# Optimization experiments

Hardware: AMD Instinct MI355X
Metric: run time of the kernel (lower is better)

The kernel has to match this reference:

```python
import jax, jax.numpy as jnp
import numpy as np

B, S, H = 4, 2048, 2048

def setup_inputs() -> dict:
    key = jax.random.key(0)
    k1, k2, k3 = jax.random.split(key, 3)
    xav_qkv = float(np.sqrt(6.0 / (H + 3 * H)))
    xav_out = float(np.sqrt(6.0 / (H + H)))
    return {
        "hidden_states": jax.random.normal(k1, (B, S, H), dtype=jnp.float32),
        "w_qkv": jax.random.uniform(k2, (3 * H, H), minval=-xav_qkv, maxval=xav_qkv, dtype=jnp.float32),
        "b_qkv": jnp.zeros((3 * H,), dtype=jnp.float32),
        "w_out": jax.random.uniform(k3, (H, H), minval=-xav_out, maxval=xav_out, dtype=jnp.float32),
        "b_out": jnp.zeros((H,), dtype=jnp.float32),
    }

def reference(hidden_states, w_qkv, b_qkv, w_out, b_out):
    Bc, Sc, Hc = hidden_states.shape
    scaling = jnp.sqrt(jnp.asarray(Hc, hidden_states.dtype))
    # qkv projection: torch Linear is x @ W^T + b
    qkv = jnp.einsum('bsh,oh->bso', hidden_states, w_qkv) + b_qkv  # [B,S,3H]
    q, k, v = jnp.split(qkv, 3, axis=-1)  # each [B,S,H]
    scores = jnp.einsum('bqh,bkh->bqk', q, k) / scaling  # [B,S,S]
    probs = jax.nn.softmax(scores, axis=-1)
    context = jnp.einsum('bqk,bkh->bqh', probs, v)  # [B,S,H]
    out = jnp.einsum('bsh,oh->bso', context, w_out) + b_out
    return out
```

## Files before the change

### kernel.cpp

```cpp
#include <hip/hip_runtime.h>
#include <cstdint>

typedef _Float16 f16;
typedef __attribute__((ext_vector_type(8))) _Float16 f16x8;
typedef __attribute__((ext_vector_type(4))) _Float16 f16x4;
typedef __attribute__((ext_vector_type(4))) float f32x4;

typedef __attribute__((address_space(1))) void gvoid_t;
typedef __attribute__((address_space(3))) void lvoid_t;

__device__ __forceinline__ void async_copy16(void* lds, const void* g) {
  __builtin_amdgcn_global_load_lds((gvoid_t*)(uintptr_t)g, (lvoid_t*)lds, 16, 0, 0);
}

#define BARRIER()   __builtin_amdgcn_s_barrier()
#define SCHEDBAR()  __builtin_amdgcn_sched_barrier(0)
#define VMCNT(n)    do { SCHEDBAR(); asm volatile("s_waitcnt vmcnt(" #n ")"); SCHEDBAR(); } while (0)

#define MFMA16(a, b, c) __builtin_amdgcn_mfma_f32_16x16x32_f16((a), (b), (c), 0, 0, 0)

template<int OUT_F16>
__device__ __forceinline__ void gemm_body(const f16* __restrict__ Ab, int lda,
                                          const f16* __restrict__ Bb, int ldb,
                                          void* __restrict__ Cz, int ldc,
                                          const float* __restrict__ bias,
                                          float scale, int K)
{
  __shared__ f16 AH0a[8192]; __shared__ f16 AH0b[8192];
  __shared__ f16 AH1a[8192]; __shared__ f16 AH1b[8192];
  __shared__ f16 BH0a[8192]; __shared__ f16 BH0b[8192];
  __shared__ f16 BH1a[8192]; __shared__ f16 BH1b[8192];

  const int tid = threadIdx.x, lane = tid & 63, wave = tid >> 6;
  const int wr = wave >> 2, wc = wave & 3;
  const int l15 = lane & 15, lk = lane >> 4;

  int lin = blockIdx.y * gridDim.x + blockIdx.x;
  const int nxy = gridDim.x * gridDim.y;
  if ((nxy & 7) == 0) lin = (lin & 7) * (nxy >> 3) + (lin >> 3);
  const int bx = lin % gridDim.x, by = lin / gridDim.x;

  const long brow = (long)by * 256, bcol = (long)bx * 256;

  const int r0  = tid >> 3;
  const int gc8 = (tid & 7) ^ (r0 & 7);
  const int sdst = wave * 512;

  const f16* gAa = Ab + (brow + r0) * (long)lda + gc8 * 8;
  const f16* gAb = gAa + 128L * lda;
  const f16* gBa = Bb + (bcol + r0) * (long)ldb + gc8 * 8;
  const f16* gBb = gBa + 128L * ldb;

#define STG(BUF, G, LD, KOFF) { \
    async_copy16(BUF + sdst,        (G) + (KOFF)); \
    async_copy16(BUF + 4096 + sdst, (G) + 64L * (LD) + (KOFF)); }

  const f16* myA0 = wr ? AH0b : AH0a;
  const f16* myA1 = wr ? AH1b : AH1a;
  const f16* myB0 = (wc & 2) ? BH0b : BH0a;
  const f16* myB1 = (wc & 2) ? BH1b : BH1a;

  const int x8   = l15 & 7;
  const int cb0  = (lk ^ x8) * 8;
  const int cb1  = ((4 | lk) ^ x8) * 8;
  const int lbA  = l15 * 64;
  const int lbB  = ((wc & 1) * 64 + l15) * 64;

#define RDA4(SRC, MP) { \
    af[0] = *(const f16x8*)&(SRC)[lbA + (2*(MP))   * 1024 + cb0]; \
    af[1] = *(const f16x8*)&(SRC)[lbA + (2*(MP))   * 1024 + cb1]; \
    af[2] = *(const f16x8*)&(SRC)[lbA + (2*(MP)+1) * 1024 + cb0]; \
    af[3] = *(const f16x8*)&(SRC)[lbA + (2*(MP)+1) * 1024 + cb1]; }

#define RDB8(SRC) { \
    bf[0][0] = *(const f16x8*)&(SRC)[lbB + 0 * 1024 + cb0]; \
    bf[1][0] = *(const f16x8*)&(SRC)[lbB + 0 * 1024 + cb1]; \
    bf[0][1] = *(const f16x8*)&(SRC)[lbB + 1 * 1024 + cb0]; \
    bf[1][1] = *(const f16x8*)&(SRC)[lbB + 1 * 1024 + cb1]; \
    bf[0][2] = *(const f16x8*)&(SRC)[lbB + 2 * 1024 + cb0]; \
    bf[1][2] = *(const f16x8*)&(SRC)[lbB + 2 * 1024 + cb1]; \
    bf[0][3] = *(const f16x8*)&(SRC)[lbB + 3 * 1024 + cb0]; \
    bf[1][3] = *(const f16x8*)&(SRC)[lbB + 3 * 1024 + cb1]; }

#define CLUSTER(MP) { \
    __builtin_amdgcn_s_setprio(1); \
    _Pragma("unroll") \
    for (int n = 0; n < 4; ++n) { \
      f32x4 t = MFMA16(af[0], bf[0][n], acc[2*(MP)][n]); \
      acc[2*(MP)][n] = MFMA16(af[1], bf[1][n], t); \
    } \
    _Pragma("unroll") \
    for (int n = 0; n < 4; ++n) { \
      f32x4 t = MFMA16(af[2], bf[0][n], acc[2*(MP)+1][n]); \
      acc[2*(MP)+1][n] = MFMA16(af[3], bf[1][n], t); \
    } \
    __builtin_amdgcn_s_setprio(0); }

  f32x4 acc[8][4] = {};
  f16x8 af[4], bf[2][4];
  const int NIT = K >> 7;

  STG(BH0a, gBa, ldb, 0);  STG(BH0b, gBb, ldb, 0);
  STG(AH0a, gAa, lda, 0);  STG(AH0b, gAb, lda, 0);
  STG(BH1a, gBa, ldb, 64);
  VMCNT(2);
  BARRIER();

  for (int J = 0; J < NIT; ++J) {
    const long k1 = 128L * J + 64;
    const long k2 = 128L * J + 128;
    const long k3 = 128L * J + 192;
    const bool st = (J + 1 < NIT);

    RDB8(myB0); RDA4(myA0, 0);
    STG(BH1b, gBb, ldb, k1);
    CLUSTER(0);
    RDA4(myA0, 1);
    STG(AH1a, gAa, lda, k1);
    CLUSTER(1);
    BARRIER();

    RDA4(myA0, 2);
    STG(AH1b, gAb, lda, k1);
    CLUSTER(2);
    RDA4(myA0, 3);
    if (st) STG(BH0a, gBa, ldb, k2);
    CLUSTER(3);
    if (st) { VMCNT(2); } else { VMCNT(0); }
    BARRIER();

    RDB8(myB1); RDA4(myA1, 0);
    if (st) STG(BH0b, gBb, ldb, k2);
    CLUSTER(0);
    RDA4(myA1, 1);
    if (st) STG(AH0a, gAa, lda, k2);
    CLUSTER(1);
    BARRIER();

    RDA4(myA1, 2);
    if (st) STG(AH0b, gAb, lda, k2);
    CLUSTER(2);
    RDA4(myA1, 3);
    if (st) STG(BH1a, gBa, ldb, k3);
    CLUSTER(3);
    if (st) VMCNT(2);
    BARRIER();
  }

#pragma unroll
  for (int m = 0; m < 8; ++m) {
#pragma unroll
    for (int n = 0; n < 4; ++n) {
      const long col = bcol + wc * 64 + n * 16 + l15;
      const float bv = bias ? bias[col] : 0.0f;
#pragma unroll
      for (int j = 0; j < 4; ++j) {
        const long row = brow + wr * 128 + m * 16 + lk * 4 + j;
        const float v = acc[m][n][j] * scale + bv;
        if (OUT_F16)
          ((f16*)Cz)[row * (long)ldc + col] = (f16)v;
        else
          ((float*)Cz)[row * (long)ldc + col] = v;
      }
    }
  }
#undef STG
#undef RDA4
#undef RDB8
#undef CLUSTER
}

template<int OUT_F16>
__global__ __launch_bounds__(512, 2)
void gemm256(const f16* __restrict__ A, int lda, long sA,
             const f16* __restrict__ B, int ldb, long sB,
             void* __restrict__ Cv, int ldc, long sC,
             const float* __restrict__ bias, float scale, int K)
{
  const int z = blockIdx.z;
  void* Cz = OUT_F16 ? (void*)((f16*)Cv + (long)z * sC)
                     : (void*)((float*)Cv + (long)z * sC);
  gemm_body<OUT_F16>(A + (long)z * sA, lda, B + (long)z * sB, ldb,
                     Cz, ldc, bias, scale, K);
}

__global__ __launch_bounds__(512, 2)
void gemm_sv(const f16* __restrict__ QKV, const f16* __restrict__ Wouth,
             f16* __restrict__ SCH, f16* __restrict__ VWT, float inv_sqrt_h)
{
  const int z = blockIdx.z;
  const long sQ = 2048L * 6144, sS = 2048L * 2048;
  if (z < 4) {
    gemm_body<1>(QKV + z * sQ, 6144, QKV + 2048 + z * sQ, 6144,
                 SCH + z * sS, 2048, nullptr, inv_sqrt_h, 2048);
  } else {
    const int zz = z - 4;
    gemm_body<1>(Wouth, 2048, QKV + 4096 + zz * sQ, 6144,
                 VWT + zz * sS, 2048, nullptr, 1.0f, 2048);
  }
}

__global__ void cast_all(const float* __restrict__ x,     f16* __restrict__ xh,
                         const float* __restrict__ wq,    f16* __restrict__ wqh,
                         const float* __restrict__ wo,    f16* __restrict__ woh)
{
  const int b = blockIdx.x;
  const float* in; f16* out; long n; int b0, nb;
  if (b < 2048)      { in = x;  out = xh;  n = 16777216L; b0 = 0;    nb = 2048; }
  else if (b < 3584) { in = wq; out = wqh; n = 12582912L; b0 = 2048; nb = 1536; }
  else               { in = wo; out = woh; n = 4194304L;  b0 = 3584; nb = 512;  }
  long i = ((long)(b - b0) * 256 + threadIdx.x) * 4;
  const long stride = (long)nb * 256 * 4;
  for (; i < n; i += stride) {
    const float4 v = *reinterpret_cast<const float4*>(in + i);
    f16x4 h;
    h.x = (f16)v.x; h.y = (f16)v.y; h.z = (f16)v.z; h.w = (f16)v.w;
    *reinterpret_cast<f16x4*>(out + i) = h;
  }
}

__global__ __launch_bounds__(256)
void softmax_rows(f16* __restrict__ scores) {
  const long row = blockIdx.x;
  f16* s = scores + row * 2048;
  const int tid = threadIdx.x;
  const int lane = tid & 63;
  const int wave = tid >> 6;

  const f16x8 hv = *reinterpret_cast<const f16x8*>(s + tid * 8);
  float v[8];
  float sum = 0.f;
#pragma unroll
  for (int j = 0; j < 8; ++j) { v[j] = __expf((float)hv[j]); sum += v[j]; }
#pragma unroll
  for (int off = 32; off >= 1; off >>= 1) sum += __shfl_xor(sum, off);
  __shared__ float red[4];
  if (lane == 0) red[wave] = sum;
  __syncthreads();
  const float inv = 1.0f / (red[0] + red[1] + red[2] + red[3]);

  f16x8 h;
#pragma unroll
  for (int j = 0; j < 8; ++j) h[j] = (f16)(v[j] * inv);
  *reinterpret_cast<f16x8*>(s + tid * 8) = h;
}

extern "C" void kernel_launch(void* const* d_in, const int* in_sizes, int n_in,
                              void* d_out, int out_size, void* d_ws, size_t ws_size,
                              hipStream_t stream) {
  const float* x     = (const float*)d_in[0];
  const float* w_qkv = (const float*)d_in[1];
  const float* b_qkv = (const float*)d_in[2];
  const float* w_out = (const float*)d_in[3];
  const float* b_out = (const float*)d_in[4];
  float* out = (float*)d_out;

  char* ws = (char*)d_ws;
  f16*   Xh    = (f16*)(ws + 0);
  f16*   Wqkvh = (f16*)(ws + 33554432L);
  f16*   Wouth = (f16*)(ws + 58720256L);
  f16*   QKV   = (f16*)(ws + 67108864L);
  f16*   SCH   = (f16*)(ws + 167772160L);
  f16*   VWT   = (f16*)(ws + 234881024L);

  const float inv_sqrt_h = 0.022097086912079608f;

  cast_all<<<4096, 256, 0, stream>>>(x, Xh, w_qkv, Wqkvh, w_out, Wouth);

  gemm256<1><<<dim3(24, 32, 1), 512, 0, stream>>>(
      Xh, 2048, 0, Wqkvh, 2048, 0, QKV, 6144, 0, b_qkv, 1.0f, 2048);

  gemm_sv<<<dim3(8, 8, 8), 512, 0, stream>>>(QKV, Wouth, SCH, VWT, inv_sqrt_h);

  softmax_rows<<<8192, 256, 0, stream>>>(SCH);

  gemm256<0><<<dim3(8, 8, 4), 512, 0, stream>>>(
      SCH, 2048, 2048L * 2048, VWT, 2048, 2048L * 2048,
      out, 2048, 2048L * 2048, b_out, 1.0f, 2048);
}
```

Baseline: 433.8 us.

## Fuse softmax into score GEMM epilogue with atomic row sums and deferred normalization

```diff
diff --git a/kernel.cpp b/kernel.cpp
--- a/kernel.cpp
+++ b/kernel.cpp
@@ -19,18 +19,22 @@
 
 #define MFMA16(a, b, c) __builtin_amdgcn_mfma_f32_16x16x32_f16((a), (b), (c), 0, 0, 0)
 
-template<int OUT_F16>
-__device__ __forceinline__ void gemm_body(const f16* __restrict__ Ab, int lda,
+struct Smem {
+  f16 AH0a[8192]; f16 AH0b[8192];
+  f16 AH1a[8192]; f16 AH1b[8192];
+  f16 BH0a[8192]; f16 BH0b[8192];
+  f16 BH1a[8192]; f16 BH1b[8192];
+};
+
+template<int EPI>
+__device__ __forceinline__ void gemm_body(Smem& sm,
+                                          const f16* __restrict__ Ab, int lda,
                                           const f16* __restrict__ Bb, int ldb,
                                           void* __restrict__ Cz, int ldc,
                                           const float* __restrict__ bias,
+                                          float* __restrict__ rs,
                                           float scale, int K)
 {
-  __shared__ f16 AH0a[8192]; __shared__ f16 AH0b[8192];
-  __shared__ f16 AH1a[8192]; __shared__ f16 AH1b[8192];
-  __shared__ f16 BH0a[8192]; __shared__ f16 BH0b[8192];
-  __shared__ f16 BH1a[8192]; __shared__ f16 BH1b[8192];
-
   const int tid = threadIdx.x, lane = tid & 63, wave = tid >> 6;
   const int wr = wave >> 2, wc = wave & 3;
   const int l15 = lane & 15, lk = lane >> 4;
@@ -55,10 +59,10 @@
     async_copy16(BUF + sdst,        (G) + (KOFF)); \
     async_copy16(BUF + 4096 + sdst, (G) + 64L * (LD) + (KOFF)); }
 
-  const f16* myA0 = wr ? AH0b : AH0a;
-  const f16* myA1 = wr ? AH1b : AH1a;
-  const f16* myB0 = (wc & 2) ? BH0b : BH0a;
-  const f16* myB1 = (wc & 2) ? BH1b : BH1a;
+  const f16* myA0 = wr ? sm.AH0b : sm.AH0a;
+  const f16* myA1 = wr ? sm.AH1b : sm.AH1a;
+  const f16* myB0 = (wc & 2) ? sm.BH0b : sm.BH0a;
+  const f16* myB1 = (wc & 2) ? sm.BH1b : sm.BH1a;
 
   const int x8   = l15 & 7;
   const int cb0  = (lk ^ x8) * 8;
@@ -100,9 +104,9 @@
   f16x8 af[4], bf[2][4];
   const int NIT = K >> 7;
 
-  STG(BH0a, gBa, ldb, 0);  STG(BH0b, gBb, ldb, 0);
-  STG(AH0a, gAa, lda, 0);  STG(AH0b, gAb, lda, 0);
-  STG(BH1a, gBa, ldb, 64);
+  STG(sm.BH0a, gBa, ldb, 0);  STG(sm.BH0b, gBb, ldb, 0);
+  STG(sm.AH0a, gAa, lda, 0);  STG(sm.AH0b, gAb, lda, 0);
+  STG(sm.BH1a, gBa, ldb, 64);
   VMCNT(2);
   BARRIER();
 
@@ -113,35 +117,35 @@
     const bool st = (J + 1 < NIT);
 
     RDB8(myB0); RDA4(myA0, 0);
-    STG(BH1b, gBb, ldb, k1);
+    STG(sm.BH1b, gBb, ldb, k1);
     CLUSTER(0);
     RDA4(myA0, 1);
-    STG(AH1a, gAa, lda, k1);
+    STG(sm.AH1a, gAa, lda, k1);
     CLUSTER(1);
     BARRIER();
 
     RDA4(myA0, 2);
-    STG(AH1b, gAb, lda, k1);
+    STG(sm.AH1b, gAb, lda, k1);
     CLUSTER(2);
     RDA4(myA0, 3);
-    if (st) STG(BH0a, gBa, ldb, k2);
+    if (st) STG(sm.BH0a, gBa, ldb, k2);
     CLUSTER(3);
     if (st) { VMCNT(2); } else { VMCNT(0); }
     BARRIER();
 
     RDB8(myB1); RDA4(myA1, 0);
-    if (st) STG(BH0b, gBb, ldb, k2);
+    if (st) STG(sm.BH0b, gBb, ldb, k2);
     CLUSTER(0);
     RDA4(myA1, 1);
-    if (st) STG(AH0a, gAa, lda, k2);
+    if (st) STG(sm.AH0a, gAa, lda, k2);
     CLUSTER(1);
     BARRIER();
 
     RDA4(myA1, 2);
-    if (st) STG(AH0b, gAb, lda, k2);
+    if (st) STG(sm.AH0b, gAb, lda, k2);
     CLUSTER(2);
     RDA4(myA1, 3);
-    if (st) STG(BH1a, gBa, ldb, k3);
+    if (st) STG(sm.BH1a, gBa, ldb, k3);
     CLUSTER(3);
     if (st) VMCNT(2);
     BARRIER();
@@ -150,17 +154,30 @@
 #pragma unroll
   for (int m = 0; m < 8; ++m) {
 #pragma unroll
-    for (int n = 0; n < 4; ++n) {
-      const long col = bcol + wc * 64 + n * 16 + l15;
-      const float bv = bias ? bias[col] : 0.0f;
+    for (int j = 0; j < 4; ++j) {
+      const long row = brow + wr * 128 + m * 16 + lk * 4 + j;
+      float inv = 0.f, part = 0.f;
+      if (EPI == 3) inv = 1.0f / rs[row];
 #pragma unroll
-      for (int j = 0; j < 4; ++j) {
-        const long row = brow + wr * 128 + m * 16 + lk * 4 + j;
-        const float v = acc[m][n][j] * scale + bv;
-        if (OUT_F16)
-          ((f16*)Cz)[row * (long)ldc + col] = (f16)v;
-        else
-          ((float*)Cz)[row * (long)ldc + col] = v;
+      for (int n = 0; n < 4; ++n) {
+        const long col = bcol + wc * 64 + n * 16 + l15;
+        const float a = acc[m][n][j];
+        if (EPI == 1) {
+          ((f16*)Cz)[row * (long)ldc + col] = (f16)(a * scale + (bias ? bias[col] : 0.f));
+        } else if (EPI == 2) {
+          const float e = __expf(a * scale);
+          part += e;
+          ((f16*)Cz)[row * (long)ldc + col] = (f16)e;
+        } else {
+          ((float*)Cz)[row * (long)ldc + col] = a * inv + bias[col];
+        }
+      }
+      if (EPI == 2) {
+        part += __shfl_xor(part, 1, 16);
+        part += __shfl_xor(part, 2, 16);
+        part += __shfl_xor(part, 4, 16);
+        part += __shfl_xor(part, 8, 16);
+        if (l15 == 0) atomicAdd(&rs[row], part);
       }
     }
   }
@@ -170,41 +187,57 @@
 #undef CLUSTER
 }
 
-template<int OUT_F16>
 __global__ __launch_bounds__(512, 2)
-void gemm256(const f16* __restrict__ A, int lda, long sA,
-             const f16* __restrict__ B, int ldb, long sB,
-             void* __restrict__ Cv, int ldc, long sC,
-             const float* __restrict__ bias, float scale, int K)
-{
-  const int z = blockIdx.z;
-  void* Cz = OUT_F16 ? (void*)((f16*)Cv + (long)z * sC)
-                     : (void*)((float*)Cv + (long)z * sC);
-  gemm_body<OUT_F16>(A + (long)z * sA, lda, B + (long)z * sB, ldb,
-                     Cz, ldc, bias, scale, K);
+void gemm_qkv(const f16* __restrict__ Xh, const f16* __restrict__ Wqkvh,
+              f16* __restrict__ QKV, const float* __restrict__ b_qkv)
+{
+  __shared__ Smem sm;
+  gemm_body<1>(sm, Xh, 2048, Wqkvh, 2048, QKV, 6144, b_qkv, nullptr, 1.0f, 2048);
 }
 
 __global__ __launch_bounds__(512, 2)
 void gemm_sv(const f16* __restrict__ QKV, const f16* __restrict__ Wouth,
-             f16* __restrict__ SCH, f16* __restrict__ VWT, float inv_sqrt_h)
-{
+             f16* __restrict__ SCH, f16* __restrict__ VWT,
+             float* __restrict__ RS, float inv_sqrt_h)
+{
+  __shared__ Smem sm;
   const int z = blockIdx.z;
   const long sQ = 2048L * 6144, sS = 2048L * 2048;
   if (z < 4) {
-    gemm_body<1>(QKV + z * sQ, 6144, QKV + 2048 + z * sQ, 6144,
-                 SCH + z * sS, 2048, nullptr, inv_sqrt_h, 2048);
+    gemm_body<2>(sm, QKV + z * sQ, 6144, QKV + 2048 + z * sQ, 6144,
+                 SCH + z * sS, 2048, nullptr, RS + z * 2048, inv_sqrt_h, 2048);
   } else {
     const int zz = z - 4;
-    gemm_body<1>(Wouth, 2048, QKV + 4096 + zz * sQ, 6144,
-                 VWT + zz * sS, 2048, nullptr, 1.0f, 2048);
-  }
+    gemm_body<1>(sm, Wouth, 2048, QKV + 4096 + zz * sQ, 6144,
+                 VWT + zz * sS, 2048, nullptr, nullptr, 1.0f, 2048);
+  }
+}
+
+__global__ __launch_bounds__(512, 2)
+void gemm_out(const f16* __restrict__ SCH, const f16* __restrict__ VWT,
+              float* __restrict__ out, float* __restrict__ RS,
+              const float* __restrict__ b_out)
+{
+  __shared__ Smem sm;
+  const int z = blockIdx.z;
+  const long sS = 2048L * 2048;
+  gemm_body<3>(sm, SCH + z * sS, 2048, VWT + z * sS, 2048,
+               out + z * sS, 2048, b_out, RS + z * 2048, 1.0f, 2048);
 }
 
 __global__ void cast_all(const float* __restrict__ x,     f16* __restrict__ xh,
                          const float* __restrict__ wq,    f16* __restrict__ wqh,
-                         const float* __restrict__ wo,    f16* __restrict__ woh)
+                         const float* __restrict__ wo,    f16* __restrict__ woh,
+                         float* __restrict__ rs)
 {
   const int b = blockIdx.x;
+  if (b >= 4096) {
+    float4 z4 = {0.f, 0.f, 0.f, 0.f};
+    float* p = rs + (long)(b - 4096) * 2048 + threadIdx.x * 8;
+    *reinterpret_cast<float4*>(p) = z4;
+    *reinterpret_cast<float4*>(p + 4) = z4;
+    return;
+  }
   const float* in; f16* out; long n; int b0, nb;
   if (b < 2048)      { in = x;  out = xh;  n = 16777216L; b0 = 0;    nb = 2048; }
   else if (b < 3584) { in = wq; out = wqh; n = 12582912L; b0 = 2048; nb = 1536; }
@@ -219,32 +252,6 @@
   }
 }
 
-__global__ __launch_bounds__(256)
-void softmax_rows(f16* __restrict__ scores) {
-  const long row = blockIdx.x;
-  f16* s = scores + row * 2048;
-  const int tid = threadIdx.x;
-  const int lane = tid & 63;
-  const int wave = tid >> 6;
-
-  const f16x8 hv = *reinterpret_cast<const f16x8*>(s + tid * 8);
-  float v[8];
-  float sum = 0.f;
-#pragma unroll
-  for (int j = 0; j < 8; ++j) { v[j] = __expf((float)hv[j]); sum += v[j]; }
-#pragma unroll
-  for (int off = 32; off >= 1; off >>= 1) sum += __shfl_xor(sum, off);
-  __shared__ float red[4];
-  if (lane == 0) red[wave] = sum;
-  __syncthreads();
-  const float inv = 1.0f / (red[0] + red[1] + red[2] + red[3]);
-
-  f16x8 h;
-#pragma unroll
-  for (int j = 0; j < 8; ++j) h[j] = (f16)(v[j] * inv);
-  *reinterpret_cast<f16x8*>(s + tid * 8) = h;
-}
-
 extern "C" void kernel_launch(void* const* d_in, const int* in_sizes, int n_in,
                               void* d_out, int out_size, void* d_ws, size_t ws_size,
                               hipStream_t stream) {
@@ -260,21 +267,17 @@
   f16*   Wqkvh = (f16*)(ws + 33554432L);
   f16*   Wouth = (f16*)(ws + 58720256L);
   f16*   QKV   = (f16*)(ws + 67108864L);
-  f16*   SCH   = (f16*)(ws + 167772160L);
+  float* RS    = (float*)(ws + 167772160L);
   f16*   VWT   = (f16*)(ws + 234881024L);
+  f16*   SCH   = Xh;
 
   const float inv_sqrt_h = 0.022097086912079608f;
 
-  cast_all<<<4096, 256, 0, stream>>>(x, Xh, w_qkv, Wqkvh, w_out, Wouth);
-
-  gemm256<1><<<dim3(24, 32, 1), 512, 0, stream>>>(
-      Xh, 2048, 0, Wqkvh, 2048, 0, QKV, 6144, 0, b_qkv, 1.0f, 2048);
-
-  gemm_sv<<<dim3(8, 8, 8), 512, 0, stream>>>(QKV, Wouth, SCH, VWT, inv_sqrt_h);
-
-  softmax_rows<<<8192, 256, 0, stream>>>(SCH);
-
-  gemm256<0><<<dim3(8, 8, 4), 512, 0, stream>>>(
-      SCH, 2048, 2048L * 2048, VWT, 2048, 2048L * 2048,
-      out, 2048, 2048L * 2048, b_out, 1.0f, 2048);
-}
+  cast_all<<<4100, 256, 0, stream>>>(x, Xh, w_qkv, Wqkvh, w_out, Wouth, RS);
+
+  gemm_qkv<<<dim3(24, 32, 1), 512, 0, stream>>>(Xh, Wqkvh, QKV, b_qkv);
+
+  gemm_sv<<<dim3(8, 8, 8), 512, 0, stream>>>(QKV, Wouth, SCH, VWT, RS, inv_sqrt_h);
+
+  gemm_out<<<dim3(8, 8, 4), 512, 0, stream>>>(SCH, VWT, out, RS, b_out);
+}
```

New measurement: 446.2 us. +2.8%, slower.
